# Kernel optimization log

Measured on AMD Instinct MI355X. Metric: run time of the kernel, lower is better.

## Reference

```python
import jax, jax.numpy as jnp
import numpy as np


def setup_inputs() -> dict:
    key = jax.random.key(0)
    ks = jax.random.split(key, 10)
    B, C, H = 128, 768, 12
    d = C // H
    t_h = t_w = 8
    s_h = s_w = 16
    Nt = t_h * t_w * 2          # 128 template tokens
    Ns = s_h * s_w + 4          # 260 search tokens
    N = Nt + Ns                 # 388
    s = 0.02
    return {
        "x": jax.random.normal(ks[0], (B, N, C), jnp.float32),
        "mem": jax.random.normal(ks[1], (B, H, d, d), jnp.float32),
        "z": jnp.ones((B, H, d, 1), jnp.float32),
        "qkv_w": jax.random.normal(ks[2], (3 * C, C), jnp.float32) * s,
        "qkv_b": jnp.zeros((3 * C,), jnp.float32),
        "proj_w": jax.random.normal(ks[3], (C, C), jnp.float32) * s,
        "proj_b": jnp.zeros((C,), jnp.float32),
        "memk_w": jax.random.normal(ks[4], (C, C), jnp.float32) * s,
        "memk_b": jnp.zeros((C,), jnp.float32),
        "memv_w": jax.random.normal(ks[5], (C, C), jnp.float32) * s,
        "memv_b": jnp.zeros((C,), jnp.float32),
        "betas": jax.random.normal(ks[6], (1, H, 1, d), jnp.float32),
        "t_h": t_h, "t_w": t_w, "s_h": s_h, "s_w": s_w,
    }


def reference(x, mem, z, qkv_w, qkv_b, proj_w, proj_b,
              memk_w, memk_b, memv_w, memv_b, betas,
              t_h, t_w, s_h, s_w):
    B, N, C = x.shape
    H = betas.shape[1]
    d = C // H
    Nt = t_h * t_w * 2
    Ns = s_h * s_w + 4
    scale = 1.0 / jnp.sqrt(jnp.float32(d))

    qkv = x @ qkv_w.T + qkv_b                       # [B,N,3C]
    qkv = qkv.reshape(B, N, 3, C)
    q_f, k_f, v_f = qkv[:, :, 0], qkv[:, :, 1], qkv[:, :, 2]  # [B,N,C]

    def heads(t):  # [B,N,C] -> [B,H,N,d]
        return t.reshape(B, -1, H, d).transpose(0, 2, 1, 3)

    q, k, v = heads(q_f), heads(k_f), heads(v_f)

    # memory k/v projections act on the raw (C-dim) search split of k,v
    k_s_mem = heads(k_f[:, Nt:, :] @ memk_w.T + memk_b)  # [B,H,Ns,d]
    v_s_mem = heads(v_f[:, Nt:, :] @ memv_w.T + memv_b)  # [B,H,Ns,d]

    q_mt, q_s = q[:, :, :Nt], q[:, :, Nt:]
    k_mt = k[:, :, :Nt]
    v_mt = v[:, :, :Nt]

    # template self-attention (q_mt only attends to k_mt)
    attn_mt = jax.nn.softmax(jnp.einsum('bhqd,bhkd->bhqk', q_mt, k_mt) * scale, axis=-1)
    x_mt = jnp.einsum('bhqk,bhkd->bhqd', attn_mt, v_mt)          # [B,H,Nt,d]
    x_mt = x_mt.transpose(0, 2, 1, 3).reshape(B, Nt, C)

    # search attends to full sequence
    attn_s = jax.nn.softmax(jnp.einsum('bhqd,bhkd->bhqk', q_s, k) * scale, axis=-1)
    x_s = jnp.einsum('bhqk,bhkd->bhqd', attn_s, v)               # [B,H,Ns,d]

    # linear-attention memory read (ELU feature map)
    sigma_q = jax.nn.elu(q_s) + 1.0                              # [B,H,Ns,d]
    att_mem = (sigma_q @ mem) / (sigma_q @ z)                    # [B,H,Ns,d]

    # delta-rule memory update
    sigma_k = jax.nn.elu(k_s_mem) + 1.0                          # [B,H,Ns,d]
    zz = jnp.sum(sigma_k, axis=-2, keepdims=True).swapaxes(-2, -1)  # [B,H,d,1]
    pred = (sigma_k @ mem) / (sigma_k @ z)                       # [B,H,Ns,d]
    mem_new = mem + jnp.einsum('bhnd,bhne->bhde', sigma_k, v_s_mem - pred)
    z_new = z + zz

    beta = jax.nn.sigmoid(betas)                                 # [1,H,1,d]
    x_s = beta * att_mem + (1.0 - beta) * x_s
    x_s = x_s.transpose(0, 2, 1, 3).reshape(B, Ns, C)

    out = jnp.concatenate([x_mt, x_s], axis=1) @ proj_w.T + proj_b
    return out, mem_new, z_new
```

## Files before the change

kernel.cpp:

```cpp
#include <hip/hip_runtime.h>

typedef unsigned short u16;
typedef __attribute__((ext_vector_type(8))) short  vbf8;
typedef __attribute__((ext_vector_type(4))) float  vf4;

#define B_   128
#define N_   388
#define NT   128
#define NS   260
#define C_   768
#define H_   12
#define D_   64
#define K3   2304

#define QKV_LEN  114425856ll
#define KSM_LEN  25559040ll
#define CAT_LEN  38141952ll
#define MEM_LEN  6291456ll

#define SPS  288
#define SPL  296

#define WOFF_QKV  0ll
#define WOFF_MEMK 1769472ll
#define WOFF_MEMV 2359296ll
#define WOFF_PROJ 2949120ll
#define WTOT     3538944ll
__device__ __align__(16) u16 g_wbf[3538944];

__device__ __forceinline__ float bf2f(u16 u) {
    union { unsigned int i; float f; } v; v.i = ((unsigned int)u) << 16; return v.f;
}
__device__ __forceinline__ u16 f2bf(float f) {
    union { float f; unsigned int i; } v; v.f = f;
    unsigned int r = v.i + 0x7fffu + ((v.i >> 16) & 1u);
    return (u16)(r >> 16);
}
__device__ __forceinline__ float elu1(float x) { return x > 0.f ? x + 1.f : __expf(x); }

__device__ __forceinline__ void gload_lds16(const u16* g, u16* l) {
    __builtin_amdgcn_global_load_lds(
        (const __attribute__((address_space(1))) unsigned int*)g,
        (__attribute__((address_space(3))) unsigned int*)l, 16, 0, 0);
}

__global__ __launch_bounds__(256) void convert_all(
    const float* __restrict__ x, u16* __restrict__ x_bf,
    const float* __restrict__ s0, const float* __restrict__ s1,
    const float* __restrict__ s2, const float* __restrict__ s3)
{
    int bid = blockIdx.x;
    if (bid < 2048) {
        long long i0 = ((long long)bid * 256 + threadIdx.x) * 8;
        long long stride = 2048ll * 256 * 8;
        for (long long i = i0; i < CAT_LEN; i += stride) {
            float4 a = *(const float4*)(x + i);
            float4 b = *(const float4*)(x + i + 4);
            ushort4 u1; u1.x = f2bf(a.x); u1.y = f2bf(a.y); u1.z = f2bf(a.z); u1.w = f2bf(a.w);
            ushort4 u2; u2.x = f2bf(b.x); u2.y = f2bf(b.y); u2.z = f2bf(b.z); u2.w = f2bf(b.w);
            *(ushort4*)(x_bf + i)     = u1;
            *(ushort4*)(x_bf + i + 4) = u2;
        }
    } else {
        long long i = ((long long)(bid - 2048) * 256 + threadIdx.x) * 8;
        if (i >= WTOT) return;
        const float* src; long long off;
        if (i < WOFF_MEMK)      { src = s0; off = i; }
        else if (i < WOFF_MEMV) { src = s1; off = i - WOFF_MEMK; }
        else if (i < WOFF_PROJ) { src = s2; off = i - WOFF_MEMV; }
        else                    { src = s3; off = i - WOFF_PROJ; }
        float4 a = *(const float4*)(src + off);
        float4 b = *(const float4*)(src + off + 4);
        ushort4 u1; u1.x = f2bf(a.x); u1.y = f2bf(a.y); u1.z = f2bf(a.z); u1.w = f2bf(a.w);
        ushort4 u2; u2.x = f2bf(b.x); u2.y = f2bf(b.y); u2.z = f2bf(b.z); u2.w = f2bf(b.w);
        *(ushort4*)(g_wbf + i)     = u1;
        *(ushort4*)(g_wbf + i + 4) = u2;
    }
}

__global__ __launch_bounds__(256) void memT_kernel(
    const float* __restrict__ memin, u16* __restrict__ memT)
{
    __shared__ float ml[64 * 65];
    int bh = blockIdx.x, t = threadIdx.x;
    const float* src = memin + (long long)bh * 4096;
#pragma unroll
    for (int i = 0; i < 16; i++) {
        int idx = i * 256 + t;
        ml[(idx >> 6) * 65 + (idx & 63)] = src[idx];
    }
    __syncthreads();
    u16* dst = memT + (long long)bh * 4096;
#pragma unroll
    for (int i = 0; i < 16; i++) {
        int o = i * 256 + t;
        int dout = o >> 6, din = o & 63;
        dst[o] = f2bf(ml[din * 65 + dout]);
    }
}

template<int CF32>
__device__ __forceinline__ void gemm_body(
    int wgid, int ngrid,
    const u16* __restrict__ A, long long off0, int rows_per_b,
    long long stride_b, long long stride_r,
    const u16* __restrict__ W, const float* __restrict__ bias,
    void* __restrict__ Cv, int Nout, int nbx)
{
    __shared__ __align__(16) u16 lds[2][2][4096];

    int t = threadIdx.x;

    int wg = (wgid & 7) * (ngrid >> 3) + (wgid >> 3);
    int m0 = (wg / nbx) * 128;
    int n0 = (wg % nbx) * 128;

    int lane = t & 63, w = t >> 6;
    int w512 = w * 512;

    int srow  = t >> 2;
    int scol  = (((t & 3) ^ (srow & 3))) * 8;
    long long aoff0, aoff1;
    {
        int g1 = m0 + srow, g2 = g1 + 64;
        int b1 = g1 / rows_per_b, j1 = g1 - b1 * rows_per_b;
        int b2 = g2 / rows_per_b, j2 = g2 - b2 * rows_per_b;
        aoff0 = off0 + (long long)b1 * stride_b + (long long)j1 * stride_r + scol;
        aoff1 = off0 + (long long)b2 * stride_b + (long long)j2 * stride_r + scol;
    }
    const u16* wp0 = W + (long long)(n0 + srow) * 768 + scol;
    const u16* wp1 = W + (long long)(n0 + srow + 64) * 768 + scol;

    int lr = lane & 15, kg = lane >> 4;
    int wm = w >> 1, wn = w & 1;
    int aslot = (kg ^ (lr & 3)) * 8;
    int abase = (wm * 64 + lr) * 32 + aslot;
    int bbase = (wn * 64 + lr) * 32 + aslot;

    vf4 acc[4][4];
#pragma unroll
    for (int i = 0; i < 4; i++)
#pragma unroll
        for (int j = 0; j < 4; j++) acc[i][j] = vf4{0.f, 0.f, 0.f, 0.f};

    auto stage = [&](int buf, int kt) {
        gload_lds16(A + aoff0 + kt, &lds[buf][0][w512]);
        gload_lds16(A + aoff1 + kt, &lds[buf][0][2048 + w512]);
        gload_lds16(wp0 + kt,       &lds[buf][1][w512]);
        gload_lds16(wp1 + kt,       &lds[buf][1][2048 + w512]);
    };

    stage(0, 0);
    __syncthreads();

    int cur = 0;
    for (int kt = 0; kt < 768; kt += 32) {
        if (kt != 736) stage(cur ^ 1, kt + 32);

        vbf8 af[4], bf[4];
#pragma unroll
        for (int f = 0; f < 4; f++) {
            af[f] = *(const vbf8*)&lds[cur][0][abase + f * 512];
            bf[f] = *(const vbf8*)&lds[cur][1][bbase + f * 512];
        }
#pragma unroll
        for (int i = 0; i < 4; i++)
#pragma unroll
            for (int j = 0; j < 4; j++)
                acc[i][j] = __builtin_amdgcn_mfma_f32_16x16x32_bf16(
                    af[i], bf[j], acc[i][j], 0, 0, 0);

        __syncthreads();
        cur ^= 1;
    }

    if (!CF32) {
        u16* ct = &lds[0][0][0];
#pragma unroll
        for (int i = 0; i < 4; i++)
#pragma unroll
            for (int j = 0; j < 4; j++) {
                int col = wn * 64 + j * 16 + lr;
                float bb = bias[n0 + col];
#pragma unroll
                for (int r = 0; r < 4; r++)
                    ct[(wm * 64 + i * 16 + kg * 4 + r) * 128 + col] =
                        f2bf(acc[i][j][r] + bb);
            }
        __syncthreads();
        int col0 = (t & 15) * 8;
#pragma unroll
        for (int rr = 0; rr < 8; rr++) {
            int row_l = rr * 16 + (t >> 4);
            vbf8 v = *(const vbf8*)&ct[row_l * 128 + col0];
            *(vbf8*)((u16*)Cv + (long long)(m0 + row_l) * Nout + n0 + col0) = v;
        }
    } else {
        float* cf = (float*)&lds[0][0][0];
#pragma unroll
        for (int p = 0; p < 2; p++) {
            if (wm == p) {
#pragma unroll
                for (int i = 0; i < 4; i++)
#pragma unroll
                    for (int j = 0; j < 4; j++) {
                        int col = wn * 64 + j * 16 + lr;
                        float bb = bias[n0 + col];
#pragma unroll
                        for (int r = 0; r < 4; r++)
                            cf[(i * 16 + kg * 4 + r) * 128 + col] =
                                acc[i][j][r] + bb;
                    }
            }
            __syncthreads();
            int col0 = (t & 15) * 8;
#pragma unroll
            for (int rr = 0; rr < 4; rr++) {
                int row_l = rr * 16 + (t >> 4);
                float4 v0 = *(const float4*)&cf[row_l * 128 + col0];
                float4 v1 = *(const float4*)&cf[row_l * 128 + col0 + 4];
                float* dst = (float*)Cv + (long long)(m0 + p * 64 + row_l) * Nout + n0 + col0;
                *(float4*)dst = v0;
                *(float4*)(dst + 4) = v1;
            }
            __syncthreads();
        }
    }
}

template<int CF32>
__global__ __launch_bounds__(256) void gemm_mfma(
    const u16* __restrict__ A, long long off0, int rows_per_b,
    long long stride_b, long long stride_r,
    long long w_off, const float* __restrict__ bias,
    void* __restrict__ Cv, int Nout, int nbx)
{
    gemm_body<CF32>(blockIdx.x, gridDim.x, A, off0, rows_per_b, stride_b,
                    stride_r, g_wbf + w_off, bias, Cv, Nout, nbx);
}

__global__ __launch_bounds__(256) void gemm_mfma_dual(
    const u16* __restrict__ A, long long off0a, long long off0b,
    int rows_per_b, long long stride_b, long long stride_r,
    long long w_offa, long long w_offb,
    const float* __restrict__ biasa, const float* __restrict__ biasb,
    void* __restrict__ Cva, void* __restrict__ Cvb, int Nout, int nbx, int half)
{
    int bid = blockIdx.x;
    if (bid < half)
        gemm_body<0>(bid, half, A, off0a, rows_per_b, stride_b, stride_r,
                     g_wbf + w_offa, biasa, Cva, Nout, nbx);
    else
        gemm_body<0>(bid - half, half, A, off0b, rows_per_b, stride_b, stride_r,
                     g_wbf + w_offb, biasb, Cvb, Nout, nbx);
}

#define SKP 416
#define VTS 424
__global__ __launch_bounds__(512) void attn_fused(
    const u16* __restrict__ qkv, const u16* __restrict__ memT,
    const float* __restrict__ zin, const float* __restrict__ betas,
    u16* __restrict__ concat)
{
    __shared__ __align__(16) u16 Kl[SKP * 64];
    __shared__ __align__(16) u16 Vt[64 * VTS];
    __shared__ __align__(16) u16 Pl[8][16 * 40];
    __shared__ float red[8][16];

    int bh = blockIdx.x;
    int b = bh / H_, h = bh % H_;
    int t = threadIdx.x, lane = t & 63, w = t >> 6;
    int lr = lane & 15, q4 = lane >> 4;

    {
        int key0 = t >> 3;
        int d0 = (t & 7) * 8;
        for (int kp = 0; kp < SKP; kp += 64) {
            int key = kp + key0;
            if (key < SKP) {
                vbf8 kv, vv;
#pragma unroll
                for (int u = 0; u < 8; u++) { ((short*)&kv)[u] = 0; ((short*)&vv)[u] = 0; }
                if (key < N_) {
                    const u16* base = qkv + ((long long)(b * N_ + key)) * K3 + h * D_;
                    kv = *(const vbf8*)(base + C_ + d0);
                    vv = *(const vbf8*)(base + 2 * C_ + d0);
                }
                *(vbf8*)((char*)Kl + ((key * 128 + d0 * 2) ^ ((key & 7) << 4))) = kv;
#pragma unroll
                for (int u = 0; u < 8; u++) Vt[(d0 + u) * VTS + key] = ((u16*)&vv)[u];
            }
        }
    }
    __syncthreads();

    const float* zp = zin + bh * 64;
    const u16* mtb = memT + (long long)bh * 4096;

    for (int s = w; s < 17; s += 8) {
        int qtok = NT + s * 16 + lr;
        if (qtok > N_ - 1) qtok = N_ - 1;
        const u16* qbase = qkv + ((long long)(b * N_ + qtok)) * K3 + h * D_;
        vbf8 qf0 = *(const vbf8*)(qbase + q4 * 8);
        vbf8 qf1 = *(const vbf8*)(qbase + 32 + q4 * 8);

        vbf8 qs0, qs1;
#pragma unroll
        for (int j = 0; j < 8; j++) {
            ((u16*)&qs0)[j] = f2bf(bf2f(((u16*)&qf0)[j]) * 0.125f);
            ((u16*)&qs1)[j] = f2bf(bf2f(((u16*)&qf1)[j]) * 0.125f);
        }

        vf4 S[13][2];
#pragma unroll
        for (int kt = 0; kt < 13; kt++) {
#pragma unroll
            for (int ks = 0; ks < 2; ks++) {
                int krow = kt * 32 + ks * 16 + lr;
                int swz = (krow & 7) << 4;
                vbf8 b0 = *(const vbf8*)((char*)Kl + ((krow * 128 + q4 * 16) ^ swz));
                vbf8 b1 = *(const vbf8*)((char*)Kl + ((krow * 128 + 64 + q4 * 16) ^ swz));
                vf4 z4 = vf4{0.f, 0.f, 0.f, 0.f};
                vf4 sv = __builtin_amdgcn_mfma_f32_16x16x32_bf16(qs0, b0, z4, 0, 0, 0);
                S[kt][ks] = __builtin_amdgcn_mfma_f32_16x16x32_bf16(qs1, b1, sv, 0, 0, 0);
            }
        }
#pragma unroll
        for (int ks = 0; ks < 2; ks++)
#pragma unroll
            for (int r = 0; r < 4; r++)
                if (ks * 16 + lr >= 4) S[12][ks][r] = -1e30f;

        float mx[4];
#pragma unroll
        for (int r = 0; r < 4; r++) mx[r] = S[0][0][r];
#pragma unroll
        for (int kt = 0; kt < 13; kt++)
#pragma unroll
            for (int ks = 0; ks < 2; ks++)
#pragma unroll
                for (int r = 0; r < 4; r++) mx[r] = fmaxf(mx[r], S[kt][ks][r]);
#pragma unroll
        for (int off = 1; off <= 8; off <<= 1)
#pragma unroll
            for (int r = 0; r < 4; r++) mx[r] = fmaxf(mx[r], __shfl_xor(mx[r], off));

        float l[4] = {0.f, 0.f, 0.f, 0.f};
#pragma unroll
        for (int kt = 0; kt < 13; kt++)
#pragma unroll
            for (int ks = 0; ks < 2; ks++)
#pragma unroll
                for (int r = 0; r < 4; r++) {
                    float p = __expf(S[kt][ks][r] - mx[r]);
                    S[kt][ks][r] = p;
                    l[r] += p;
                }
#pragma unroll
        for (int off = 1; off <= 8; off <<= 1)
#pragma unroll
            for (int r = 0; r < 4; r++) l[r] += __shfl_xor(l[r], off);

        vf4 accO[4];
#pragma unroll
        for (int dc = 0; dc < 4; dc++) accO[dc] = vf4{0.f, 0.f, 0.f, 0.f};
#pragma unroll
        for (int kt = 0; kt < 13; kt++) {
            u16* pw = Pl[w];
#pragma unroll
            for (int ks = 0; ks < 2; ks++)
#pragma unroll
                for (int r = 0; r < 4; r++)
                    pw[(q4 * 4 + r) * 40 + ks * 16 + lr] = f2bf(S[kt][ks][r]);
            vbf8 pf = *(const vbf8*)&Pl[w][lr * 40 + q4 * 8];
#pragma unroll
            for (int dc = 0; dc < 4; dc++) {
                vbf8 vf_ = *(const vbf8*)&Vt[(dc * 16 + lr) * VTS + kt * 32 + q4 * 8];
                accO[dc] = __builtin_amdgcn_mfma_f32_16x16x32_bf16(pf, vf_, accO[dc], 0, 0, 0);
            }
        }

        float invl[4];
#pragma unroll
        for (int r = 0; r < 4; r++) invl[r] = 1.f / l[r];

        vbf8 sq0, sq1;
        float dpart = 0.f;
#pragma unroll
        for (int j = 0; j < 8; j++) {
            float s0 = elu1(bf2f(((u16*)&qf0)[j]));
            float s1 = elu1(bf2f(((u16*)&qf1)[j]));
            ((u16*)&sq0)[j] = f2bf(s0);
            ((u16*)&sq1)[j] = f2bf(s1);
            dpart += s0 * zp[q4 * 8 + j] + s1 * zp[32 + q4 * 8 + j];
        }
        dpart += __shfl_xor(dpart, 16);
        dpart += __shfl_xor(dpart, 32);
        if (q4 == 0) red[w][lr] = dpart;

        vf4 am[4];
#pragma unroll
        for (int dc = 0; dc < 4; dc++) {
            vbf8 b0 = *(const vbf8*)(mtb + (dc * 16 + lr) * 64 + q4 * 8);
            vbf8 b1 = *(const vbf8*)(mtb + (dc * 16 + lr) * 64 + 32 + q4 * 8);
            vf4 z4 = vf4{0.f, 0.f, 0.f, 0.f};
            vf4 a = __builtin_amdgcn_mfma_f32_16x16x32_bf16(sq0, b0, z4, 0, 0, 0);
            am[dc] = __builtin_amdgcn_mfma_f32_16x16x32_bf16(sq1, b1, a, 0, 0, 0);
        }
        float den[4];
#pragma unroll
        for (int r = 0; r < 4; r++) den[r] = 1.f / red[w][q4 * 4 + r];

#pragma unroll
        for (int dc = 0; dc < 4; dc++) {
            float bb = betas[h * D_ + dc * 16 + lr];
            float beta = 1.f / (1.f + __expf(-bb));
#pragma unroll
            for (int r = 0; r < 4; r++) {
                int qs = s * 16 + q4 * 4 + r;
                if (qs < NS) {
                    float o = beta * (am[dc][r] * den[r]) +
                              (1.f - beta) * (accO[dc][r] * invl[r]);
                    concat[((long long)(b * N_ + NT + qs)) * C_ + h * D_ + dc * 16 + lr] = f2bf(o);
                }
            }
        }
    }

    if (w > 0) {
        for (int m = w - 1; m < 8; m += 7) {
            int qtok = m * 16 + lr;
            const u16* qbase = qkv + ((long long)(b * N_ + qtok)) * K3 + h * D_;
            vbf8 qf0 = *(const vbf8*)(qbase + q4 * 8);
            vbf8 qf1 = *(const vbf8*)(qbase + 32 + q4 * 8);
            vbf8 qs0, qs1;
#pragma unroll
            for (int j = 0; j < 8; j++) {
                ((u16*)&qs0)[j] = f2bf(bf2f(((u16*)&qf0)[j]) * 0.125f);
                ((u16*)&qs1)[j] = f2bf(bf2f(((u16*)&qf1)[j]) * 0.125f);
            }

            vf4 S4[4][2];
#pragma unroll
            for (int kt = 0; kt < 4; kt++) {
#pragma unroll
                for (int ks = 0; ks < 2; ks++) {
                    int krow = kt * 32 + ks * 16 + lr;
                    int swz = (krow & 7) << 4;
                    vbf8 b0 = *(const vbf8*)((char*)Kl + ((krow * 128 + q4 * 16) ^ swz));
                    vbf8 b1 = *(const vbf8*)((char*)Kl + ((krow * 128 + 64 + q4 * 16) ^ swz));
                    vf4 z4 = vf4{0.f, 0.f, 0.f, 0.f};
                    vf4 sv = __builtin_amdgcn_mfma_f32_16x16x32_bf16(qs0, b0, z4, 0, 0, 0);
                    S4[kt][ks] = __builtin_amdgcn_mfma_f32_16x16x32_bf16(qs1, b1, sv, 0, 0, 0);
                }
            }

            float mx[4];
#pragma unroll
            for (int r = 0; r < 4; r++) mx[r] = S4[0][0][r];
#pragma unroll
            for (int kt = 0; kt < 4; kt++)
#pragma unroll
                for (int ks = 0; ks < 2; ks++)
#pragma unroll
                    for (int r = 0; r < 4; r++) mx[r] = fmaxf(mx[r], S4[kt][ks][r]);
#pragma unroll
            for (int off = 1; off <= 8; off <<= 1)
#pragma unroll
                for (int r = 0; r < 4; r++) mx[r] = fmaxf(mx[r], __shfl_xor(mx[r], off));

            float l[4] = {0.f, 0.f, 0.f, 0.f};
#pragma unroll
            for (int kt = 0; kt < 4; kt++)
#pragma unroll
                for (int ks = 0; ks < 2; ks++)
#pragma unroll
                    for (int r = 0; r < 4; r++) {
                        float p = __expf(S4[kt][ks][r] - mx[r]);
                        S4[kt][ks][r] = p;
                        l[r] += p;
                    }
#pragma unroll
            for (int off = 1; off <= 8; off <<= 1)
#pragma unroll
                for (int r = 0; r < 4; r++) l[r] += __shfl_xor(l[r], off);

            vf4 accO[4];
#pragma unroll
            for (int dc = 0; dc < 4; dc++) accO[dc] = vf4{0.f, 0.f, 0.f, 0.f};
#pragma unroll
            for (int kt = 0; kt < 4; kt++) {
                u16* pw = Pl[w];
#pragma unroll
                for (int ks = 0; ks < 2; ks++)
#pragma unroll
                    for (int r = 0; r < 4; r++)
                        pw[(q4 * 4 + r) * 40 + ks * 16 + lr] = f2bf(S4[kt][ks][r]);
                vbf8 pf = *(const vbf8*)&Pl[w][lr * 40 + q4 * 8];
#pragma unroll
                for (int dc = 0; dc < 4; dc++) {
                    vbf8 vf_ = *(const vbf8*)&Vt[(dc * 16 + lr) * VTS + kt * 32 + q4 * 8];
                    accO[dc] = __builtin_amdgcn_mfma_f32_16x16x32_bf16(pf, vf_, accO[dc], 0, 0, 0);
                }
            }

            float invl[4];
#pragma unroll
            for (int r = 0; r < 4; r++) invl[r] = 1.f / l[r];

            int qt0 = m * 16;
#pragma unroll
            for (int dc = 0; dc < 4; dc++)
#pragma unroll
                for (int r = 0; r < 4; r++) {
                    int row = qt0 + q4 * 4 + r;
                    concat[((long long)(b * N_ + row)) * C_ + h * D_ + dc * 16 + lr] =
                        f2bf(accO[dc][r] * invl[r]);
                }
        }
    }
}

__global__ __launch_bounds__(512) void sigma_pred_mem(
    const u16* __restrict__ ksm, const u16* __restrict__ vsm,
    const u16* __restrict__ memT, const float* __restrict__ zin,
    const float* __restrict__ memin, float* __restrict__ mem_out,
    float* __restrict__ z_out)
{
    __shared__ __align__(16) u16 sigL[64][SPL];
    __shared__ __align__(16) u16 wL[64][SPL];
    __shared__ float red[8][16];
    __shared__ float zpart[8][64];
    __shared__ float zlds[64];

    int bh = blockIdx.x;
    int b = bh / H_, h = bh % H_;
    int t = threadIdx.x, lane = t & 63, w = t >> 6;
    int lr = lane & 15, q4 = lane >> 4;

    if (t < 64) zlds[t] = zin[bh * 64 + t];
    __syncthreads();

    const u16* mtb = memT + (long long)bh * 4096;
    float zacc[16];
#pragma unroll
    for (int j = 0; j < 16; j++) zacc[j] = 0.f;

    for (int s = w; s < 18; s += 8) {
        int n0 = s * 16;
        int nrow = n0 + lr;
        bool vrow = nrow < NS;
        int nclamp = vrow ? nrow : NS - 1;
        const u16* kbase = ksm + ((long long)(b * NS + nclamp)) * C_ + h * D_;
        vbf8 k0 = *(const vbf8*)(kbase + q4 * 8);
        vbf8 k1 = *(const vbf8*)(kbase + 32 + q4 * 8);

        vbf8 sq0, sq1;
        float dpart = 0.f;
#pragma unroll
        for (int j = 0; j < 8; j++) {
            float s0 = vrow ? elu1(bf2f(((u16*)&k0)[j])) : 0.f;
            float s1 = vrow ? elu1(bf2f(((u16*)&k1)[j])) : 0.f;
            u16 b0 = f2bf(s0), b1 = f2bf(s1);
            ((u16*)&sq0)[j] = b0;
            ((u16*)&sq1)[j] = b1;
            zacc[j]     += s0;
            zacc[8 + j] += s1;
            dpart += s0 * zlds[q4 * 8 + j] + s1 * zlds[32 + q4 * 8 + j];
            sigL[q4 * 8 + j][n0 + lr]      = b0;
            sigL[32 + q4 * 8 + j][n0 + lr] = b1;
        }
        dpart += __shfl_xor(dpart, 16);
        dpart += __shfl_xor(dpart, 32);
        if (q4 == 0) red[w][lr] = dpart;

        vf4 am[4];
#pragma unroll
        for (int dc = 0; dc < 4; dc++) {
            vbf8 b0 = *(const vbf8*)(mtb + (dc * 16 + lr) * 64 + q4 * 8);
            vbf8 b1 = *(const vbf8*)(mtb + (dc * 16 + lr) * 64 + 32 + q4 * 8);
            vf4 z4 = vf4{0.f, 0.f, 0.f, 0.f};
            vf4 a = __builtin_amdgcn_mfma_f32_16x16x32_bf16(sq0, b0, z4, 0, 0, 0);
            am[dc] = __builtin_amdgcn_mfma_f32_16x16x32_bf16(sq1, b1, a, 0, 0, 0);
        }
        float rden[4];
#pragma unroll
        for (int r = 0; r < 4; r++) rden[r] = 1.f / red[w][q4 * 4 + r];

#pragma unroll
        for (int dc = 0; dc < 4; dc++) {
            int e = dc * 16 + lr;
#pragma unroll
            for (int r = 0; r < 4; r++) {
                int nn = n0 + q4 * 4 + r;
                float wv = 0.f;
                if (nn < NS) {
                    float pv = am[dc][r] * rden[r];
                    wv = bf2f(vsm[((long long)(b * NS + nn)) * C_ + h * D_ + e]) - pv;
                }
                wL[e][n0 + q4 * 4 + r] = f2bf(wv);
            }
        }
    }

#pragma unroll
    for (int off = 1; off <= 8; off <<= 1)
#pragma unroll
        for (int j = 0; j < 16; j++) zacc[j] += __shfl_xor(zacc[j], off);
    if (lr == 0) {
#pragma unroll
        for (int j = 0; j < 8; j++) {
            zpart[w][q4 * 8 + j]      = zacc[j];
            zpart[w][32 + q4 * 8 + j] = zacc[8 + j];
        }
    }
    __syncthreads();

    if (t < 64) {
        float tot = 0.f;
#pragma unroll
        for (int ww = 0; ww < 8; ww++) tot += zpart[ww][t];
        z_out[bh * 64 + t] = zlds[t] + tot;
    }

    long long mb = (long long)bh * 4096;
#pragma unroll
    for (int p = 0; p < 2; p++) {
        int tid2 = w * 2 + p;
        int i = tid2 >> 2, j = tid2 & 3;
        vf4 acc = vf4{0.f, 0.f, 0.f, 0.f};
#pragma unroll
        for (int kt = 0; kt < SPS; kt += 32) {
            vbf8 af = *(const vbf8*)&sigL[i * 16 + lr][kt + q4 * 8];
            vbf8 bf = *(const vbf8*)&wL[j * 16 + lr][kt + q4 * 8];
            acc = __builtin_amdgcn_mfma_f32_16x16x32_bf16(af, bf, acc, 0, 0, 0);
        }
        int e = j * 16 + lr;
#pragma unroll
        for (int r = 0; r < 4; r++) {
            int dd = i * 16 + q4 * 4 + r;
            mem_out[mb + dd * 64 + e] = memin[mb + dd * 64 + e] + acc[r];
        }
    }
}

extern "C" void kernel_launch(void* const* d_in, const int* in_sizes, int n_in,
                              void* d_out, int out_size, void* d_ws, size_t ws_size,
                              hipStream_t stream)
{
    const float* x      = (const float*)d_in[0];
    const float* mem    = (const float*)d_in[1];
    const float* z      = (const float*)d_in[2];
    const float* qkv_w  = (const float*)d_in[3];
    const float* qkv_b  = (const float*)d_in[4];
    const float* proj_w = (const float*)d_in[5];
    const float* proj_b = (const float*)d_in[6];
    const float* memk_w = (const float*)d_in[7];
    const float* memk_b = (const float*)d_in[8];
    const float* memv_w = (const float*)d_in[9];
    const float* memv_b = (const float*)d_in[10];
    const float* betas  = (const float*)d_in[11];

    u16* ws     = (u16*)d_ws;
    u16* qkv    = ws;
    u16* ksm    = qkv + QKV_LEN;
    u16* vsm    = ksm + KSM_LEN;
    u16* concat = vsm + KSM_LEN;

    float* out     = (float*)d_out;
    float* mem_out = out + CAT_LEN;
    float* z_out   = mem_out + MEM_LEN;

    u16* x_bf = concat;
    u16* memT = (u16*)out;

    convert_all<<<dim3(2048 + 1728), dim3(256), 0, stream>>>(
        x, x_bf, qkv_w, memk_w, memv_w, proj_w);
    memT_kernel<<<dim3(B_ * H_), dim3(256), 0, stream>>>(mem, memT);

    gemm_mfma<0><<<dim3(6984), dim3(256), 0, stream>>>(
        x_bf, 0ll, 49664, 0ll, 768ll, WOFF_QKV, qkv_b, qkv, K3, 18);
    gemm_mfma_dual<<<dim3(3120), dim3(256), 0, stream>>>(
        qkv, (long long)(NT * K3 + C_), (long long)(NT * K3 + 2 * C_),
        NS, (long long)N_ * K3, (long long)K3,
        WOFF_MEMK, WOFF_MEMV, memk_b, memv_b, ksm, vsm, C_, 6, 1560);
    attn_fused<<<dim3(B_ * H_), dim3(512), 0, stream>>>(
        qkv, memT, z, betas, concat);
    sigma_pred_mem<<<dim3(B_ * H_), dim3(512), 0, stream>>>(
        ksm, vsm, memT, z, mem, mem_out, z_out);
    gemm_mfma<1><<<dim3(2328), dim3(256), 0, stream>>>(
        concat, 0ll, 49664, 0ll, 768ll, WOFF_PROJ, proj_b, out, C_, 6);
}
```

Baseline: 858.4 us.

## Merge prep kernels, use exp2 softmax with folded log2e, add MFMA priority hints

The memory transpose is folded into the conversion kernel as extra blocks, removing one launch. The softmax in the attention kernel now multiplies q by 0.125·log2(e) so it can use exp2f in place of __expf. s_setprio is raised around the MFMA sections so waves issuing matrix ops get scheduling priority. Conversion stores are widened to 16-byte vector writes. The extra blocks enlarge the prep grid, and the bf16 rounding of the pre-scaled q changes slightly.

```diff
diff --git a/kernel.cpp b/kernel.cpp
--- a/kernel.cpp
+++ b/kernel.cpp
@@ -21,6 +21,8 @@
 #define SPS  288
 #define SPL  296
 
+#define SM2  0.18033688f
+
 #define WOFF_QKV  0ll
 #define WOFF_MEMK 1769472ll
 #define WOFF_MEMV 2359296ll
@@ -44,25 +46,33 @@
         (__attribute__((address_space(3))) unsigned int*)l, 16, 0, 0);
 }
 
-__global__ __launch_bounds__(256) void convert_all(
+__device__ __forceinline__ vbf8 pack8(float4 a, float4 b) {
+    vbf8 v;
+    ((u16*)&v)[0] = f2bf(a.x); ((u16*)&v)[1] = f2bf(a.y);
+    ((u16*)&v)[2] = f2bf(a.z); ((u16*)&v)[3] = f2bf(a.w);
+    ((u16*)&v)[4] = f2bf(b.x); ((u16*)&v)[5] = f2bf(b.y);
+    ((u16*)&v)[6] = f2bf(b.z); ((u16*)&v)[7] = f2bf(b.w);
+    return v;
+}
+
+__global__ __launch_bounds__(256) void prep_kernel(
     const float* __restrict__ x, u16* __restrict__ x_bf,
     const float* __restrict__ s0, const float* __restrict__ s1,
-    const float* __restrict__ s2, const float* __restrict__ s3)
+    const float* __restrict__ s2, const float* __restrict__ s3,
+    const float* __restrict__ memin, u16* __restrict__ memT)
 {
     int bid = blockIdx.x;
+    int t = threadIdx.x;
     if (bid < 2048) {
-        long long i0 = ((long long)bid * 256 + threadIdx.x) * 8;
+        long long i0 = ((long long)bid * 256 + t) * 8;
         long long stride = 2048ll * 256 * 8;
         for (long long i = i0; i < CAT_LEN; i += stride) {
             float4 a = *(const float4*)(x + i);
             float4 b = *(const float4*)(x + i + 4);
-            ushort4 u1; u1.x = f2bf(a.x); u1.y = f2bf(a.y); u1.z = f2bf(a.z); u1.w = f2bf(a.w);
-            ushort4 u2; u2.x = f2bf(b.x); u2.y = f2bf(b.y); u2.z = f2bf(b.z); u2.w = f2bf(b.w);
-            *(ushort4*)(x_bf + i)     = u1;
-            *(ushort4*)(x_bf + i + 4) = u2;
-        }
-    } else {
-        long long i = ((long long)(bid - 2048) * 256 + threadIdx.x) * 8;
+            *(vbf8*)(x_bf + i) = pack8(a, b);
+        }
+    } else if (bid < 2048 + 1728) {
+        long long i = ((long long)(bid - 2048) * 256 + t) * 8;
         if (i >= WTOT) return;
         const float* src; long long off;
         if (i < WOFF_MEMK)      { src = s0; off = i; }
@@ -71,31 +81,24 @@
         else                    { src = s3; off = i - WOFF_PROJ; }
         float4 a = *(const float4*)(src + off);
         float4 b = *(const float4*)(src + off + 4);
-        ushort4 u1; u1.x = f2bf(a.x); u1.y = f2bf(a.y); u1.z = f2bf(a.z); u1.w = f2bf(a.w);
-        ushort4 u2; u2.x = f2bf(b.x); u2.y = f2bf(b.y); u2.z = f2bf(b.z); u2.w = f2bf(b.w);
-        *(ushort4*)(g_wbf + i)     = u1;
-        *(ushort4*)(g_wbf + i + 4) = u2;
-    }
-}
-
-__global__ __launch_bounds__(256) void memT_kernel(
-    const float* __restrict__ memin, u16* __restrict__ memT)
-{
-    __shared__ float ml[64 * 65];
-    int bh = blockIdx.x, t = threadIdx.x;
-    const float* src = memin + (long long)bh * 4096;
-#pragma unroll
-    for (int i = 0; i < 16; i++) {
-        int idx = i * 256 + t;
-        ml[(idx >> 6) * 65 + (idx & 63)] = src[idx];
-    }
-    __syncthreads();
-    u16* dst = memT + (long long)bh * 4096;
-#pragma unroll
-    for (int i = 0; i < 16; i++) {
-        int o = i * 256 + t;
-        int dout = o >> 6, din = o & 63;
-        dst[o] = f2bf(ml[din * 65 + dout]);
+        *(vbf8*)(g_wbf + i) = pack8(a, b);
+    } else {
+        __shared__ float ml[64 * 65];
+        int bh = bid - (2048 + 1728);
+        const float* src = memin + (long long)bh * 4096;
+#pragma unroll
+        for (int i = 0; i < 16; i++) {
+            int idx = i * 256 + t;
+            ml[(idx >> 6) * 65 + (idx & 63)] = src[idx];
+        }
+        __syncthreads();
+        u16* dst = memT + (long long)bh * 4096;
+#pragma unroll
+        for (int i = 0; i < 16; i++) {
+            int o = i * 256 + t;
+            int dout = o >> 6, din = o & 63;
+            dst[o] = f2bf(ml[din * 65 + dout]);
+        }
     }
 }
 
@@ -307,11 +310,12 @@
         vbf8 qs0, qs1;
 #pragma unroll
         for (int j = 0; j < 8; j++) {
-            ((u16*)&qs0)[j] = f2bf(bf2f(((u16*)&qf0)[j]) * 0.125f);
-            ((u16*)&qs1)[j] = f2bf(bf2f(((u16*)&qf1)[j]) * 0.125f);
+            ((u16*)&qs0)[j] = f2bf(bf2f(((u16*)&qf0)[j]) * SM2);
+            ((u16*)&qs1)[j] = f2bf(bf2f(((u16*)&qf1)[j]) * SM2);
         }
 
         vf4 S[13][2];
+        __builtin_amdgcn_s_setprio(1);
 #pragma unroll
         for (int kt = 0; kt < 13; kt++) {
 #pragma unroll
@@ -325,6 +329,7 @@
                 S[kt][ks] = __builtin_amdgcn_mfma_f32_16x16x32_bf16(qs1, b1, sv, 0, 0, 0);
             }
         }
+        __builtin_amdgcn_s_setprio(0);
 #pragma unroll
         for (int ks = 0; ks < 2; ks++)
 #pragma unroll
@@ -352,7 +357,7 @@
             for (int ks = 0; ks < 2; ks++)
 #pragma unroll
                 for (int r = 0; r < 4; r++) {
-                    float p = __expf(S[kt][ks][r] - mx[r]);
+                    float p = exp2f(S[kt][ks][r] - mx[r]);
                     S[kt][ks][r] = p;
                     l[r] += p;
                 }
@@ -364,6 +369,7 @@
         vf4 accO[4];
 #pragma unroll
         for (int dc = 0; dc < 4; dc++) accO[dc] = vf4{0.f, 0.f, 0.f, 0.f};
+        __builtin_amdgcn_s_setprio(1);
 #pragma unroll
         for (int kt = 0; kt < 13; kt++) {
             u16* pw = Pl[w];
@@ -379,6 +385,7 @@
                 accO[dc] = __builtin_amdgcn_mfma_f32_16x16x32_bf16(pf, vf_, accO[dc], 0, 0, 0);
             }
         }
+        __builtin_amdgcn_s_setprio(0);
 
         float invl[4];
 #pragma unroll
@@ -399,6 +406,7 @@
         if (q4 == 0) red[w][lr] = dpart;
 
         vf4 am[4];
+        __builtin_amdgcn_s_setprio(1);
 #pragma unroll
         for (int dc = 0; dc < 4; dc++) {
             vbf8 b0 = *(const vbf8*)(mtb + (dc * 16 + lr) * 64 + q4 * 8);
@@ -407,6 +415,7 @@
             vf4 a = __builtin_amdgcn_mfma_f32_16x16x32_bf16(sq0, b0, z4, 0, 0, 0);
             am[dc] = __builtin_amdgcn_mfma_f32_16x16x32_bf16(sq1, b1, a, 0, 0, 0);
         }
+        __builtin_amdgcn_s_setprio(0);
         float den[4];
 #pragma unroll
         for (int r = 0; r < 4; r++) den[r] = 1.f / red[w][q4 * 4 + r];
@@ -436,11 +445,12 @@
             vbf8 qs0, qs1;
 #pragma unroll
             for (int j = 0; j < 8; j++) {
-                ((u16*)&qs0)[j] = f2bf(bf2f(((u16*)&qf0)[j]) * 0.125f);
-                ((u16*)&qs1)[j] = f2bf(bf2f(((u16*)&qf1)[j]) * 0.125f);
+                ((u16*)&qs0)[j] = f2bf(bf2f(((u16*)&qf0)[j]) * SM2);
+                ((u16*)&qs1)[j] = f2bf(bf2f(((u16*)&qf1)[j]) * SM2);
             }
 
             vf4 S4[4][2];
+            __builtin_amdgcn_s_setprio(1);
 #pragma unroll
             for (int kt = 0; kt < 4; kt++) {
 #pragma unroll
@@ -454,6 +464,7 @@
                     S4[kt][ks] = __builtin_amdgcn_mfma_f32_16x16x32_bf16(qs1, b1, sv, 0, 0, 0);
                 }
             }
+            __builtin_amdgcn_s_setprio(0);
 
             float mx[4];
 #pragma unroll
@@ -476,7 +487,7 @@
                 for (int ks = 0; ks < 2; ks++)
 #pragma unroll
                     for (int r = 0; r < 4; r++) {
-                        float p = __expf(S4[kt][ks][r] - mx[r]);
+                        float p = exp2f(S4[kt][ks][r] - mx[r]);
                         S4[kt][ks][r] = p;
                         l[r] += p;
                     }
@@ -488,6 +499,7 @@
             vf4 accO[4];
 #pragma unroll
             for (int dc = 0; dc < 4; dc++) accO[dc] = vf4{0.f, 0.f, 0.f, 0.f};
+            __builtin_amdgcn_s_setprio(1);
 #pragma unroll
             for (int kt = 0; kt < 4; kt++) {
                 u16* pw = Pl[w];
@@ -503,6 +515,7 @@
                     accO[dc] = __builtin_amdgcn_mfma_f32_16x16x32_bf16(pf, vf_, accO[dc], 0, 0, 0);
                 }
             }
+            __builtin_amdgcn_s_setprio(0);
 
             float invl[4];
 #pragma unroll
@@ -674,9 +687,8 @@
     u16* x_bf = concat;
     u16* memT = (u16*)out;
 
-    convert_all<<<dim3(2048 + 1728), dim3(256), 0, stream>>>(
-        x, x_bf, qkv_w, memk_w, memv_w, proj_w);
-    memT_kernel<<<dim3(B_ * H_), dim3(256), 0, stream>>>(mem, memT);
+    prep_kernel<<<dim3(2048 + 1728 + 1536), dim3(256), 0, stream>>>(
+        x, x_bf, qkv_w, memk_w, memv_w, proj_w, mem, memT);
 
     gemm_mfma<0><<<dim3(6984), dim3(256), 0, stream>>>(
         x_bf, 0ll, 49664, 0ll, 768ll, WOFF_QKV, qkv_b, qkv, K3, 18);
```

New measurement: 866.5 us (median of 3 runs). No clear change (+0.9%).
